# Performance work log

Measured on AMD Instinct MI355X. Metric: run time of the kernel, lower is better.

Reference implementation:

```python
import jax, jax.numpy as jnp
import numpy as np

EMBED_DIM = 1024
NUM_HEADS = 16
HEAD_DIM = EMBED_DIM // NUM_HEADS


def setup_inputs() -> dict:
    key = jax.random.key(0)
    ks = jax.random.split(key, 12)
    B, S, D = 4, 2048, EMBED_DIM
    scale = 1.0 / np.sqrt(D)
    inp = {
        "query": jax.random.normal(ks[0], (B, S, D), jnp.float32),
        "key": jax.random.normal(ks[1], (B, S, D), jnp.float32),
        "value": jax.random.normal(ks[2], (B, S, D), jnp.float32),
        # nn.Linear weights: [out_features, in_features], y = x @ W.T + b
        "Wq": jax.random.normal(ks[3], (D, D), jnp.float32) * scale,
        "bq": jnp.zeros((D,), jnp.float32),
        "Wk": jax.random.normal(ks[4], (D, D), jnp.float32) * scale,
        "bk": jnp.zeros((D,), jnp.float32),
        "Wv": jax.random.normal(ks[5], (D, D), jnp.float32) * scale,
        "bv": jnp.zeros((D,), jnp.float32),
        "Wo": jax.random.normal(ks[6], (D, D), jnp.float32) * scale,
        "bo": jnp.zeros((D,), jnp.float32),
    }
    return inp


def reference(query, key, value, Wq, bq, Wk, bk, Wv, bv, Wo, bo):
    B, Sq, D = query.shape
    Sk = key.shape[1]
    H, Dh = NUM_HEADS, HEAD_DIM

    def proj(x, W, b):
        # [B,S,D] -> [B,H,S,Dh]
        y = jnp.einsum('bsd,ed->bse', x, W) + b
        return y.reshape(x.shape[0], x.shape[1], H, Dh).transpose(0, 2, 1, 3)

    q = proj(query, Wq, bq)
    k = proj(key, Wk, bk)
    v = proj(value, Wv, bv)

    # sigmoid attention (no softmax); dropout is identity in eval mode
    scores = jnp.einsum('bhqd,bhkd->bhqk', q, k) / jnp.sqrt(jnp.float32(Dh)).astype(q.dtype)
    attn = jax.nn.sigmoid(scores)
    out = jnp.einsum('bhqk,bhkd->bhqd', attn, v)

    out = out.transpose(0, 2, 1, 3).reshape(B, Sq, D)
    return jnp.einsum('bsd,ed->bse', out, Wo) + bo
```

## Files before the change

### kernel.cpp

```cpp
#include <hip/hip_runtime.h>


typedef _Float16 f16x2 __attribute__((ext_vector_type(2)));
typedef _Float16 f16x4 __attribute__((ext_vector_type(4)));
typedef _Float16 f16x8 __attribute__((ext_vector_type(8)));
typedef __fp16   h16x2 __attribute__((ext_vector_type(2)));
typedef float    f32x4 __attribute__((ext_vector_type(4)));
typedef float    f32x16 __attribute__((ext_vector_type(16)));

typedef __attribute__((address_space(3))) void* lds_vp;
typedef const __attribute__((address_space(1))) void* gbl_vp;

__device__ __forceinline__ void gld_lds16(const void* g, void* l) {
  __builtin_amdgcn_global_load_lds((gbl_vp)g, (lds_vp)l, 16, 0, 0);
}

__device__ __forceinline__ f16x8 cvt8(float4 a, float4 b) {
  return (f16x8){(_Float16)a.x, (_Float16)a.y, (_Float16)a.z, (_Float16)a.w,
                 (_Float16)b.x, (_Float16)b.y, (_Float16)b.z, (_Float16)b.w};
}

__device__ __forceinline__ f16x2 pk2(float a, float b) {
  h16x2 r = __builtin_amdgcn_cvt_pkrtz(a, b);
  return __builtin_bit_cast(f16x2, r);
}

#define BM 128
#define BN 128
#define BK 32

template <bool AF16, bool BF16, bool TRANSV, bool OUTF32>
__global__ __launch_bounds__(256) void gemm_bt(const void* __restrict__ Av,
                                               const void* __restrict__ Bv,
                                               const float* __restrict__ bias,
                                               void* __restrict__ Yv,
                                               int M, int N, int K) {
  __shared__ __align__(16) _Float16 sA[BM * BK];
  __shared__ __align__(16) _Float16 sB[BN * BK];

  const int t = threadIdx.x, lane = t & 63, wid = t >> 6;
  const int m0 = blockIdx.x * BM, n0 = blockIdx.y * BN;
  const int wm = (wid >> 1) * 64, wn = (wid & 1) * 64;
  const int lrow = lane & 15, g = lane >> 4;

  f32x4 acc[4][4] = {};

  const int arow = 16 * wid + (lane >> 2);
  const int gq = (lane & 3) ^ ((lane >> 3) & 3);
  _Float16* lA1 = sA + wid * 512;
  _Float16* lA2 = sA + 2048 + wid * 512;
  _Float16* lB1 = sB + wid * 512;
  _Float16* lB2 = sB + 2048 + wid * 512;

  const int mrow = t >> 1, mhalf = t & 1;
  const int mm = (mrow >> 1) & 3;
  const int ch_lo = mrow * 4 + ((2 * mhalf) ^ mm);
  const int ch_hi = ch_lo ^ 1;

  const _Float16* pA16a = nullptr; const _Float16* pA16b = nullptr;
  const float* pA32 = nullptr;
  if constexpr (AF16) {
    const _Float16* A = (const _Float16*)Av;
    pA16a = A + (size_t)(m0 + arow) * K + gq * 8;
    pA16b = A + (size_t)(m0 + 64 + arow) * K + gq * 8;
  } else {
    pA32 = (const float*)Av + (size_t)(m0 + mrow) * K + mhalf * 16;
  }
  const _Float16* pB16a = nullptr; const _Float16* pB16b = nullptr;
  const float* pB32 = nullptr;
  if constexpr (BF16) {
    const _Float16* B = (const _Float16*)Bv;
    pB16a = B + (size_t)(n0 + arow) * K + gq * 8;
    pB16b = B + (size_t)(n0 + 64 + arow) * K + gq * 8;
  } else {
    pB32 = (const float*)Bv + (size_t)(n0 + mrow) * K + mhalf * 16;
  }

  const int xr = g ^ ((lrow >> 1) & 3);

  for (int k0 = 0; k0 < K; k0 += BK) {
    float4 av[4], bv4[4];
    if constexpr (!AF16) {
      const float4* p = (const float4*)(pA32 + k0);
      av[0] = p[0]; av[1] = p[1]; av[2] = p[2]; av[3] = p[3];
    }
    if constexpr (!BF16) {
      const float4* p = (const float4*)(pB32 + k0);
      bv4[0] = p[0]; bv4[1] = p[1]; bv4[2] = p[2]; bv4[3] = p[3];
    }
    __syncthreads();
    if constexpr (AF16) {
      gld_lds16(pA16a + k0, lA1);
      gld_lds16(pA16b + k0, lA2);
    } else {
      *(f16x8*)(sA + ch_lo * 8) = cvt8(av[0], av[1]);
      *(f16x8*)(sA + ch_hi * 8) = cvt8(av[2], av[3]);
    }
    if constexpr (BF16) {
      gld_lds16(pB16a + k0, lB1);
      gld_lds16(pB16b + k0, lB2);
    } else {
      *(f16x8*)(sB + ch_lo * 8) = cvt8(bv4[0], bv4[1]);
      *(f16x8*)(sB + ch_hi * 8) = cvt8(bv4[2], bv4[3]);
    }
    __syncthreads();

    f16x8 af[4], bf[4];
#pragma unroll
    for (int i = 0; i < 4; i++)
      af[i] = *(const f16x8*)(sA + (wm + i * 16 + lrow) * 32 + xr * 8);
#pragma unroll
    for (int j = 0; j < 4; j++)
      bf[j] = *(const f16x8*)(sB + (wn + j * 16 + lrow) * 32 + xr * 8);
#pragma unroll
    for (int i = 0; i < 4; i++)
#pragma unroll
      for (int j = 0; j < 4; j++)
        acc[i][j] = __builtin_amdgcn_mfma_f32_16x16x32_f16(af[i], bf[j], acc[i][j], 0, 0, 0);
  }

  const int orow = g * 4, ocol = lrow;
#pragma unroll
  for (int j = 0; j < 4; j++) {
    const int col = n0 + wn + j * 16 + ocol;
    const float bv = bias[col];
#pragma unroll
    for (int i = 0; i < 4; i++) {
      const int row = m0 + wm + i * 16 + orow;
      if constexpr (TRANSV) {
        _Float16* VT = (_Float16*)Yv;
        int s = row & 2047;
        int sp = (s & ~12) | ((s & 4) << 1) | ((s & 8) >> 1);
        _Float16* dst = VT + (((size_t)(row >> 11) * 16 + (col >> 6)) * 64 + (col & 63)) * 2048 + sp;
        f16x4 v = {(_Float16)(acc[i][j][0] + bv), (_Float16)(acc[i][j][1] + bv),
                   (_Float16)(acc[i][j][2] + bv), (_Float16)(acc[i][j][3] + bv)};
        *(f16x4*)dst = v;
      } else if constexpr (OUTF32) {
        float* Y = (float*)Yv;
#pragma unroll
        for (int r = 0; r < 4; r++) Y[(size_t)(row + r) * N + col] = acc[i][j][r] + bv;
      } else {
        _Float16* Y = (_Float16*)Yv;
#pragma unroll
        for (int r = 0; r < 4; r++) Y[(size_t)(row + r) * N + col] = (_Float16)(acc[i][j][r] + bv);
      }
    }
  }
}

__global__ __launch_bounds__(256) void qkv_gemm(const _Float16* __restrict__ Xq,
                                                const _Float16* __restrict__ Xk,
                                                const _Float16* __restrict__ Xv,
                                                const _Float16* __restrict__ W,
                                                const float* __restrict__ bq,
                                                const float* __restrict__ bk,
                                                const float* __restrict__ bv,
                                                _Float16* __restrict__ Qo,
                                                _Float16* __restrict__ Ko,
                                                _Float16* __restrict__ VT) {
  __shared__ __align__(16) _Float16 sA[BM * BK];
  __shared__ __align__(16) _Float16 sB[BN * BK];

  const int t = threadIdx.x, lane = t & 63, wid = t >> 6;
  const int n0g = blockIdx.x * BN, m0 = blockIdx.y * BM;
  const int seg = blockIdx.x >> 3, n0 = n0g & 1023;
  const _Float16* A = (seg == 0) ? Xq : (seg == 1) ? Xk : Xv;
  const float* bias = (seg == 0) ? bq : (seg == 1) ? bk : bv;
  const int K = 1024;

  const int wm = (wid >> 1) * 64, wn = (wid & 1) * 64;
  const int lrow = lane & 15, g = lane >> 4;

  f32x4 acc[4][4] = {};

  const int arow = 16 * wid + (lane >> 2);
  const int gq = (lane & 3) ^ ((lane >> 3) & 3);
  _Float16* lA1 = sA + wid * 512;
  _Float16* lA2 = sA + 2048 + wid * 512;
  _Float16* lB1 = sB + wid * 512;
  _Float16* lB2 = sB + 2048 + wid * 512;

  const _Float16* pA16a = A + (size_t)(m0 + arow) * K + gq * 8;
  const _Float16* pA16b = A + (size_t)(m0 + 64 + arow) * K + gq * 8;
  const _Float16* pB16a = W + (size_t)(n0g + arow) * K + gq * 8;
  const _Float16* pB16b = W + (size_t)(n0g + 64 + arow) * K + gq * 8;

  const int xr = g ^ ((lrow >> 1) & 3);

  for (int k0 = 0; k0 < K; k0 += BK) {
    __syncthreads();
    gld_lds16(pA16a + k0, lA1);
    gld_lds16(pA16b + k0, lA2);
    gld_lds16(pB16a + k0, lB1);
    gld_lds16(pB16b + k0, lB2);
    __syncthreads();

    f16x8 af[4], bf[4];
#pragma unroll
    for (int i = 0; i < 4; i++)
      af[i] = *(const f16x8*)(sA + (wm + i * 16 + lrow) * 32 + xr * 8);
#pragma unroll
    for (int j = 0; j < 4; j++)
      bf[j] = *(const f16x8*)(sB + (wn + j * 16 + lrow) * 32 + xr * 8);
#pragma unroll
    for (int i = 0; i < 4; i++)
#pragma unroll
      for (int j = 0; j < 4; j++)
        acc[i][j] = __builtin_amdgcn_mfma_f32_16x16x32_f16(af[i], bf[j], acc[i][j], 0, 0, 0);
  }

  const int orow = g * 4, ocol = lrow;
#pragma unroll
  for (int j = 0; j < 4; j++) {
    const int col = n0 + wn + j * 16 + ocol;
    const float bvv = bias[col];
#pragma unroll
    for (int i = 0; i < 4; i++) {
      const int row = m0 + wm + i * 16 + orow;
      if (seg == 2) {
        int s = row & 2047;
        int sp = (s & ~12) | ((s & 4) << 1) | ((s & 8) >> 1);
        _Float16* dst = VT + (((size_t)(row >> 11) * 16 + (col >> 6)) * 64 + (col & 63)) * 2048 + sp;
        f16x4 v = {(_Float16)(acc[i][j][0] + bvv), (_Float16)(acc[i][j][1] + bvv),
                   (_Float16)(acc[i][j][2] + bvv), (_Float16)(acc[i][j][3] + bvv)};
        *(f16x4*)dst = v;
      } else {
        _Float16* Y = (seg == 0) ? Qo : Ko;
#pragma unroll
        for (int r = 0; r < 4; r++) Y[(size_t)(row + r) * 1024 + col] = (_Float16)(acc[i][j][r] + bvv);
      }
    }
  }
}

#define LDS_ROW 72

__global__ __launch_bounds__(256, 4) void attn_sig(const _Float16* __restrict__ Q,
                                                   const _Float16* __restrict__ K,
                                                   const _Float16* __restrict__ VT,
                                                   _Float16* __restrict__ O) {
  __shared__ __align__(16) _Float16 smem[128 * LDS_ROW];
  _Float16* sK = smem;
  _Float16* sVT = smem + 64 * LDS_ROW;

  const int t = threadIdx.x, lane = t & 63, wid = t >> 6;
  const int l31 = lane & 31, g5 = lane >> 5;
  const int b = blockIdx.z, h = blockIdx.y, q0 = blockIdx.x * 128;
  const int qw = q0 + wid * 32;

  f16x8 qf[4];
  {
    const _Float16* qp = Q + (size_t)(b * 2048 + qw + l31) * 1024 + h * 64;
#pragma unroll
    for (int dhc = 0; dhc < 4; dhc++)
      qf[dhc] = *(const f16x8*)(qp + dhc * 16 + g5 * 8) * (_Float16)-0.125f;
  }

  f32x16 oacc[2] = {};

  const int srow = t >> 2, scol = (t & 3) * 16;
  const _Float16* kbase = K + ((size_t)(b * 2048) + srow) * 1024 + h * 64 + scol;
  const _Float16* vbase = VT + ((size_t)((b * 16 + h) * 64 + srow)) * 2048 + scol;

  uint4 ka = *(const uint4*)kbase;
  uint4 kb = *(const uint4*)(kbase + 8);
  uint4 va = *(const uint4*)vbase;
  uint4 vb = *(const uint4*)(vbase + 8);

  for (int kt = 0; kt < 2048; kt += 64) {
    __syncthreads();
    *(uint4*)&sK[srow * LDS_ROW + scol] = ka;
    *(uint4*)&sK[srow * LDS_ROW + scol + 8] = kb;
    *(uint4*)&sVT[srow * LDS_ROW + scol] = va;
    *(uint4*)&sVT[srow * LDS_ROW + scol + 8] = vb;
    __syncthreads();

    const int kt2 = kt + 64;
    if (kt2 < 2048) {
      ka = *(const uint4*)(kbase + (size_t)kt2 * 1024);
      kb = *(const uint4*)(kbase + (size_t)kt2 * 1024 + 8);
      va = *(const uint4*)(vbase + kt2);
      vb = *(const uint4*)(vbase + kt2 + 8);
    }

#pragma unroll
    for (int kt32 = 0; kt32 < 2; kt32++) {
      f16x8 kf[4];
#pragma unroll
      for (int dhc = 0; dhc < 4; dhc++)
        kf[dhc] = *(const f16x8*)&sK[(kt32 * 32 + l31) * LDS_ROW + dhc * 16 + g5 * 8];

      f32x16 sacc = {};
#pragma unroll
      for (int dhc = 0; dhc < 4; dhc++)
        sacc = __builtin_amdgcn_mfma_f32_32x32x16_f16(kf[dhc], qf[dhc], sacc, 0, 0, 0);

      f16x8 pf[2];
#pragma unroll
      for (int G = 0; G < 2; G++) {
        union { f16x8 v; f16x2 h[4]; } u;
#pragma unroll
        for (int pr = 0; pr < 4; pr++) {
          float e0 = __expf(sacc[G * 8 + pr * 2 + 0]);
          float e1 = __expf(sacc[G * 8 + pr * 2 + 1]);
          u.h[pr] = pk2(__builtin_amdgcn_rcpf(1.0f + e0),
                        __builtin_amdgcn_rcpf(1.0f + e1));
        }
        pf[G] = u.v;
      }

#pragma unroll
      for (int dht = 0; dht < 2; dht++)
#pragma unroll
        for (int G = 0; G < 2; G++) {
          f16x8 vf = *(const f16x8*)&sVT[(dht * 32 + l31) * LDS_ROW + kt32 * 32 + G * 16 + g5 * 8];
          oacc[dht] = __builtin_amdgcn_mfma_f32_32x32x16_f16(vf, pf[G], oacc[dht], 0, 0, 0);
        }
    }
  }

  __syncthreads();
  _Float16* ep = smem;
#pragma unroll
  for (int dht = 0; dht < 2; dht++)
#pragma unroll
    for (int c = 0; c < 4; c++) {
      f16x4 o4 = {(_Float16)oacc[dht][4 * c + 0], (_Float16)oacc[dht][4 * c + 1],
                  (_Float16)oacc[dht][4 * c + 2], (_Float16)oacc[dht][4 * c + 3]};
      *(f16x4*)&ep[(wid * 32 + l31) * LDS_ROW + dht * 32 + c * 8 + g5 * 4] = o4;
    }
  __syncthreads();
#pragma unroll
  for (int i = 0; i < 4; i++) {
    const int q = i * 32 + (t >> 3), dhc = t & 7;
    f16x8 row = *(const f16x8*)&ep[q * LDS_ROW + dhc * 8];
    *(f16x8*)(O + (size_t)(b * 2048 + q0 + q) * 1024 + h * 64 + dhc * 8) = row;
  }
}

struct CvtArgs {
  const float* src[7];
  _Float16* dst[7];
  int n[7];
  int cnt;
};

__global__ __launch_bounds__(256) void cvt_f32_f16(CvtArgs a) {
  const int ti = blockIdx.y;
  if (ti >= a.cnt) return;
  const int i = (blockIdx.x * 256 + threadIdx.x) * 8;
  if (i >= a.n[ti]) return;
  const float4* s = (const float4*)(a.src[ti] + i);
  float4 x = s[0], y = s[1];
  *(f16x8*)(a.dst[ti] + i) = cvt8(x, y);
}

extern "C" void kernel_launch(void* const* d_in, const int* in_sizes, int n_in,
                              void* d_out, int out_size, void* d_ws, size_t ws_size,
                              hipStream_t stream) {
  const float* query = (const float*)d_in[0];
  const float* key   = (const float*)d_in[1];
  const float* value = (const float*)d_in[2];
  const float* Wq = (const float*)d_in[3];
  const float* bq = (const float*)d_in[4];
  const float* Wk = (const float*)d_in[5];
  const float* bk = (const float*)d_in[6];
  const float* Wv = (const float*)d_in[7];
  const float* bv = (const float*)d_in[8];
  const float* Wo = (const float*)d_in[9];
  const float* bo = (const float*)d_in[10];
  float* out = (float*)d_out;

  const int D = 1024, M = 8192;
  const size_t MB = 1024 * 1024;
  char* ws = (char*)d_ws;
  dim3 bb(256), ga(16, 16, 4);

  if (ws_size >= 104 * MB) {
    _Float16* Xq = (_Float16*)(ws + 0 * MB);
    _Float16* Xk = (_Float16*)(ws + 16 * MB);
    _Float16* Xv = (_Float16*)(ws + 32 * MB);
    _Float16* Qp = (_Float16*)(ws + 48 * MB);
    _Float16* Kp = (_Float16*)(ws + 64 * MB);
    _Float16* VT = (_Float16*)(ws + 80 * MB);
    _Float16* Wf = (_Float16*)(ws + 96 * MB);
    _Float16* AO = Xq;
    CvtArgs ca{};
    ca.src[0] = query; ca.dst[0] = Xq; ca.n[0] = M * D;
    ca.src[1] = key;   ca.dst[1] = Xk; ca.n[1] = M * D;
    ca.src[2] = value; ca.dst[2] = Xv; ca.n[2] = M * D;
    ca.src[3] = Wq; ca.dst[3] = Wf + 0 * 1048576; ca.n[3] = D * D;
    ca.src[4] = Wk; ca.dst[4] = Wf + 1 * 1048576; ca.n[4] = D * D;
    ca.src[5] = Wv; ca.dst[5] = Wf + 2 * 1048576; ca.n[5] = D * D;
    ca.src[6] = Wo; ca.dst[6] = Wf + 3 * 1048576; ca.n[6] = D * D;
    ca.cnt = 7;
    cvt_f32_f16<<<dim3(4096, 7), bb, 0, stream>>>(ca);
    qkv_gemm<<<dim3(24, 64), bb, 0, stream>>>(Xq, Xk, Xv, Wf, bq, bk, bv, Qp, Kp, VT);
    attn_sig<<<ga, bb, 0, stream>>>(Qp, Kp, VT, AO);
    gemm_bt<true, true, false, true><<<dim3(64, 8), bb, 0, stream>>>(AO, Wf + 3 * 1048576, bo, out, M, D, D);
  } else {
    _Float16* Qp = (_Float16*)(ws + 0 * MB);
    _Float16* Kp = (_Float16*)(ws + 16 * MB);
    _Float16* VT = (_Float16*)(ws + 32 * MB);
    _Float16* AO = (_Float16*)(ws + 48 * MB);
    gemm_bt<false, false, false, false><<<dim3(64, 8), bb, 0, stream>>>(query, Wq, bq, Qp, M, D, D);
    gemm_bt<false, false, false, false><<<dim3(64, 8), bb, 0, stream>>>(key,   Wk, bk, Kp, M, D, D);
    gemm_bt<false, false, true,  false><<<dim3(64, 8), bb, 0, stream>>>(value, Wv, bv, VT, M, D, D);
    attn_sig<<<ga, bb, 0, stream>>>(Qp, Kp, VT, AO);
    gemm_bt<true, false, false, true><<<dim3(64, 8), bb, 0, stream>>>(AO, Wo, bo, out, M, D, D);
  }
}
```

Measured before the change: 374.3 us.

## Split attention over key halves, use exp2 with prescaled Q, add MFMA priority

Splits the key dimension of the sigmoid attention into two halves, each block writing a partial output that a new add kernel sums before the output projection. Folds log2(e) into the Q scale so the sigmoid uses a raw exp2 instruction, and raises wave priority around MFMA sections. This aims to improve occupancy and balance, and trims per-element exp work. The cost is extra partial-output traffic and an additional kernel launch.

```diff
diff --git a/kernel.cpp b/kernel.cpp
--- a/kernel.cpp
+++ b/kernel.cpp
@@ -23,6 +23,16 @@
 __device__ __forceinline__ f16x2 pk2(float a, float b) {
   h16x2 r = __builtin_amdgcn_cvt_pkrtz(a, b);
   return __builtin_bit_cast(f16x2, r);
+}
+
+__device__ __forceinline__ float exp2_fast(float x) {
+#if __has_builtin(__builtin_amdgcn_exp2f)
+  return __builtin_amdgcn_exp2f(x);
+#else
+  float r;
+  asm("v_exp_f32 %0, %1" : "=v"(r) : "v"(x));
+  return r;
+#endif
 }
 
 #define BM 128
@@ -235,6 +245,7 @@
 
 #define LDS_ROW 72
 
+template <int KSPL>
 __global__ __launch_bounds__(256, 4) void attn_sig(const _Float16* __restrict__ Q,
                                                    const _Float16* __restrict__ K,
                                                    const _Float16* __restrict__ VT,
@@ -243,9 +254,14 @@
   _Float16* sK = smem;
   _Float16* sVT = smem + 64 * LDS_ROW;
 
+  constexpr int SKEY = 2048 / KSPL;
+
   const int t = threadIdx.x, lane = t & 63, wid = t >> 6;
   const int l31 = lane & 31, g5 = lane >> 5;
-  const int b = blockIdx.z, h = blockIdx.y, q0 = blockIdx.x * 128;
+  const int b = blockIdx.z, h = blockIdx.y;
+  const int qb = (KSPL == 2) ? (int)(blockIdx.x >> 1) : (int)blockIdx.x;
+  const int kh = (KSPL == 2) ? (int)(blockIdx.x & 1) : 0;
+  const int q0 = qb * 128;
   const int qw = q0 + wid * 32;
 
   f16x8 qf[4];
@@ -253,21 +269,21 @@
     const _Float16* qp = Q + (size_t)(b * 2048 + qw + l31) * 1024 + h * 64;
 #pragma unroll
     for (int dhc = 0; dhc < 4; dhc++)
-      qf[dhc] = *(const f16x8*)(qp + dhc * 16 + g5 * 8) * (_Float16)-0.125f;
+      qf[dhc] = *(const f16x8*)(qp + dhc * 16 + g5 * 8) * (_Float16)-0.18033688f;
   }
 
   f32x16 oacc[2] = {};
 
   const int srow = t >> 2, scol = (t & 3) * 16;
-  const _Float16* kbase = K + ((size_t)(b * 2048) + srow) * 1024 + h * 64 + scol;
-  const _Float16* vbase = VT + ((size_t)((b * 16 + h) * 64 + srow)) * 2048 + scol;
+  const _Float16* kbase = K + ((size_t)(b * 2048) + kh * SKEY + srow) * 1024 + h * 64 + scol;
+  const _Float16* vbase = VT + ((size_t)((b * 16 + h) * 64 + srow)) * 2048 + kh * SKEY + scol;
 
   uint4 ka = *(const uint4*)kbase;
   uint4 kb = *(const uint4*)(kbase + 8);
   uint4 va = *(const uint4*)vbase;
   uint4 vb = *(const uint4*)(vbase + 8);
 
-  for (int kt = 0; kt < 2048; kt += 64) {
+  for (int kt = 0; kt < SKEY; kt += 64) {
     __syncthreads();
     *(uint4*)&sK[srow * LDS_ROW + scol] = ka;
     *(uint4*)&sK[srow * LDS_ROW + scol + 8] = kb;
@@ -276,7 +292,7 @@
     __syncthreads();
 
     const int kt2 = kt + 64;
-    if (kt2 < 2048) {
+    if (kt2 < SKEY) {
       ka = *(const uint4*)(kbase + (size_t)kt2 * 1024);
       kb = *(const uint4*)(kbase + (size_t)kt2 * 1024 + 8);
       va = *(const uint4*)(vbase + kt2);
@@ -291,9 +307,11 @@
         kf[dhc] = *(const f16x8*)&sK[(kt32 * 32 + l31) * LDS_ROW + dhc * 16 + g5 * 8];
 
       f32x16 sacc = {};
+      __builtin_amdgcn_s_setprio(1);
 #pragma unroll
       for (int dhc = 0; dhc < 4; dhc++)
         sacc = __builtin_amdgcn_mfma_f32_32x32x16_f16(kf[dhc], qf[dhc], sacc, 0, 0, 0);
+      __builtin_amdgcn_s_setprio(0);
 
       f16x8 pf[2];
 #pragma unroll
@@ -301,14 +319,15 @@
         union { f16x8 v; f16x2 h[4]; } u;
 #pragma unroll
         for (int pr = 0; pr < 4; pr++) {
-          float e0 = __expf(sacc[G * 8 + pr * 2 + 0]);
-          float e1 = __expf(sacc[G * 8 + pr * 2 + 1]);
+          float e0 = exp2_fast(sacc[G * 8 + pr * 2 + 0]);
+          float e1 = exp2_fast(sacc[G * 8 + pr * 2 + 1]);
           u.h[pr] = pk2(__builtin_amdgcn_rcpf(1.0f + e0),
                         __builtin_amdgcn_rcpf(1.0f + e1));
         }
         pf[G] = u.v;
       }
 
+      __builtin_amdgcn_s_setprio(1);
 #pragma unroll
       for (int dht = 0; dht < 2; dht++)
 #pragma unroll
@@ -316,9 +335,11 @@
           f16x8 vf = *(const f16x8*)&sVT[(dht * 32 + l31) * LDS_ROW + kt32 * 32 + G * 16 + g5 * 8];
           oacc[dht] = __builtin_amdgcn_mfma_f32_32x32x16_f16(vf, pf[G], oacc[dht], 0, 0, 0);
         }
-    }
-  }
-
+      __builtin_amdgcn_s_setprio(0);
+    }
+  }
+
+  _Float16* Ob = O + (size_t)kh * (8192 * 1024);
   __syncthreads();
   _Float16* ep = smem;
 #pragma unroll
@@ -334,8 +355,18 @@
   for (int i = 0; i < 4; i++) {
     const int q = i * 32 + (t >> 3), dhc = t & 7;
     f16x8 row = *(const f16x8*)&ep[q * LDS_ROW + dhc * 8];
-    *(f16x8*)(O + (size_t)(b * 2048 + q0 + q) * 1024 + h * 64 + dhc * 8) = row;
-  }
+    *(f16x8*)(Ob + (size_t)(b * 2048 + q0 + q) * 1024 + h * 64 + dhc * 8) = row;
+  }
+}
+
+__global__ __launch_bounds__(256) void add_halves(const _Float16* __restrict__ a,
+                                                  const _Float16* __restrict__ b,
+                                                  _Float16* __restrict__ o, int n) {
+  const int i = (blockIdx.x * 256 + threadIdx.x) * 8;
+  if (i >= n) return;
+  f16x8 x = *(const f16x8*)(a + i);
+  f16x8 y = *(const f16x8*)(b + i);
+  *(f16x8*)(o + i) = x + y;
 }
 
 struct CvtArgs {
@@ -374,7 +405,7 @@
   const int D = 1024, M = 8192;
   const size_t MB = 1024 * 1024;
   char* ws = (char*)d_ws;
-  dim3 bb(256), ga(16, 16, 4);
+  dim3 bb(256);
 
   if (ws_size >= 104 * MB) {
     _Float16* Xq = (_Float16*)(ws + 0 * MB);
@@ -384,7 +415,9 @@
     _Float16* Kp = (_Float16*)(ws + 64 * MB);
     _Float16* VT = (_Float16*)(ws + 80 * MB);
     _Float16* Wf = (_Float16*)(ws + 96 * MB);
-    _Float16* AO = Xq;
+    _Float16* AO0 = Xq;
+    _Float16* AO1 = Xk;
+    _Float16* AO  = Xv;
     CvtArgs ca{};
     ca.src[0] = query; ca.dst[0] = Xq; ca.n[0] = M * D;
     ca.src[1] = key;   ca.dst[1] = Xk; ca.n[1] = M * D;
@@ -396,7 +429,8 @@
     ca.cnt = 7;
     cvt_f32_f16<<<dim3(4096, 7), bb, 0, stream>>>(ca);
     qkv_gemm<<<dim3(24, 64), bb, 0, stream>>>(Xq, Xk, Xv, Wf, bq, bk, bv, Qp, Kp, VT);
-    attn_sig<<<ga, bb, 0, stream>>>(Qp, Kp, VT, AO);
+    attn_sig<2><<<dim3(32, 16, 4), bb, 0, stream>>>(Qp, Kp, VT, AO0);
+    add_halves<<<dim3(4096), bb, 0, stream>>>(AO0, AO1, AO, M * D);
     gemm_bt<true, true, false, true><<<dim3(64, 8), bb, 0, stream>>>(AO, Wf + 3 * 1048576, bo, out, M, D, D);
   } else {
     _Float16* Qp = (_Float16*)(ws + 0 * MB);
@@ -406,7 +440,7 @@
     gemm_bt<false, false, false, false><<<dim3(64, 8), bb, 0, stream>>>(query, Wq, bq, Qp, M, D, D);
     gemm_bt<false, false, false, false><<<dim3(64, 8), bb, 0, stream>>>(key,   Wk, bk, Kp, M, D, D);
     gemm_bt<false, false, true,  false><<<dim3(64, 8), bb, 0, stream>>>(value, Wv, bv, VT, M, D, D);
-    attn_sig<<<ga, bb, 0, stream>>>(Qp, Kp, VT, AO);
+    attn_sig<1><<<dim3(16, 16, 4), bb, 0, stream>>>(Qp, Kp, VT, AO);
     gemm_bt<true, false, false, true><<<dim3(64, 8), bb, 0, stream>>>(AO, Wo, bo, out, M, D, D);
   }
 }
```

New measurement: 369.2 us. About the same (-1.4%).

## Double-buffer attention K/V tiles and software-pipeline PV MFMAs with exp2 sigmoid

Applied to the files above, without the earlier changes.

The sigmoid attention kernel now keeps two LDS buffers for K/VT tiles, so each tile iteration needs one barrier instead of two. The second chunk's PV MFMA is deferred into the next iteration so it can overlap the barrier and the following QK work. The exp is replaced by a raw exp2 with the log2(e) factor folded into the Q scale. This costs double the LDS and more registers, and occupancy is lowered to 3 blocks per CU.

```diff
diff --git a/kernel.cpp b/kernel.cpp
--- a/kernel.cpp
+++ b/kernel.cpp
@@ -23,6 +23,16 @@
 __device__ __forceinline__ f16x2 pk2(float a, float b) {
   h16x2 r = __builtin_amdgcn_cvt_pkrtz(a, b);
   return __builtin_bit_cast(f16x2, r);
+}
+
+__device__ __forceinline__ float exp2_fast(float x) {
+#if __has_builtin(__builtin_amdgcn_exp2f)
+  return __builtin_amdgcn_exp2f(x);
+#else
+  float r;
+  asm("v_exp_f32 %0, %1" : "=v"(r) : "v"(x));
+  return r;
+#endif
 }
 
 #define BM 128
@@ -234,26 +244,26 @@
 }
 
 #define LDS_ROW 72
-
-__global__ __launch_bounds__(256, 4) void attn_sig(const _Float16* __restrict__ Q,
+#define TILE_E (64 * LDS_ROW)
+
+__global__ __launch_bounds__(256, 3) void attn_sig(const _Float16* __restrict__ Q,
                                                    const _Float16* __restrict__ K,
                                                    const _Float16* __restrict__ VT,
                                                    _Float16* __restrict__ O) {
-  __shared__ __align__(16) _Float16 smem[128 * LDS_ROW];
-  _Float16* sK = smem;
-  _Float16* sVT = smem + 64 * LDS_ROW;
+  __shared__ __align__(16) _Float16 smem[4 * TILE_E];
 
   const int t = threadIdx.x, lane = t & 63, wid = t >> 6;
   const int l31 = lane & 31, g5 = lane >> 5;
   const int b = blockIdx.z, h = blockIdx.y, q0 = blockIdx.x * 128;
   const int qw = q0 + wid * 32;
+  const int NT = 32;
 
   f16x8 qf[4];
   {
     const _Float16* qp = Q + (size_t)(b * 2048 + qw + l31) * 1024 + h * 64;
 #pragma unroll
     for (int dhc = 0; dhc < 4; dhc++)
-      qf[dhc] = *(const f16x8*)(qp + dhc * 16 + g5 * 8) * (_Float16)-0.125f;
+      qf[dhc] = *(const f16x8*)(qp + dhc * 16 + g5 * 8) * (_Float16)-0.18033688f;
   }
 
   f32x16 oacc[2] = {};
@@ -262,62 +272,110 @@
   const _Float16* kbase = K + ((size_t)(b * 2048) + srow) * 1024 + h * 64 + scol;
   const _Float16* vbase = VT + ((size_t)((b * 16 + h) * 64 + srow)) * 2048 + scol;
 
-  uint4 ka = *(const uint4*)kbase;
-  uint4 kb = *(const uint4*)(kbase + 8);
-  uint4 va = *(const uint4*)vbase;
-  uint4 vb = *(const uint4*)(vbase + 8);
-
-  for (int kt = 0; kt < 2048; kt += 64) {
-    __syncthreads();
-    *(uint4*)&sK[srow * LDS_ROW + scol] = ka;
-    *(uint4*)&sK[srow * LDS_ROW + scol + 8] = kb;
-    *(uint4*)&sVT[srow * LDS_ROW + scol] = va;
-    *(uint4*)&sVT[srow * LDS_ROW + scol + 8] = vb;
-    __syncthreads();
-
-    const int kt2 = kt + 64;
-    if (kt2 < 2048) {
-      ka = *(const uint4*)(kbase + (size_t)kt2 * 1024);
-      kb = *(const uint4*)(kbase + (size_t)kt2 * 1024 + 8);
-      va = *(const uint4*)(vbase + kt2);
-      vb = *(const uint4*)(vbase + kt2 + 8);
-    }
-
-#pragma unroll
-    for (int kt32 = 0; kt32 < 2; kt32++) {
-      f16x8 kf[4];
-#pragma unroll
-      for (int dhc = 0; dhc < 4; dhc++)
-        kf[dhc] = *(const f16x8*)&sK[(kt32 * 32 + l31) * LDS_ROW + dhc * 16 + g5 * 8];
-
-      f32x16 sacc = {};
-#pragma unroll
-      for (int dhc = 0; dhc < 4; dhc++)
-        sacc = __builtin_amdgcn_mfma_f32_32x32x16_f16(kf[dhc], qf[dhc], sacc, 0, 0, 0);
-
-      f16x8 pf[2];
-#pragma unroll
-      for (int G = 0; G < 2; G++) {
-        union { f16x8 v; f16x2 h[4]; } u;
-#pragma unroll
-        for (int pr = 0; pr < 4; pr++) {
-          float e0 = __expf(sacc[G * 8 + pr * 2 + 0]);
-          float e1 = __expf(sacc[G * 8 + pr * 2 + 1]);
-          u.h[pr] = pk2(__builtin_amdgcn_rcpf(1.0f + e0),
-                        __builtin_amdgcn_rcpf(1.0f + e1));
-        }
-        pf[G] = u.v;
-      }
-
-#pragma unroll
-      for (int dht = 0; dht < 2; dht++)
-#pragma unroll
-        for (int G = 0; G < 2; G++) {
-          f16x8 vf = *(const f16x8*)&sVT[(dht * 32 + l31) * LDS_ROW + kt32 * 32 + G * 16 + g5 * 8];
-          oacc[dht] = __builtin_amdgcn_mfma_f32_32x32x16_f16(vf, pf[G], oacc[dht], 0, 0, 0);
-        }
-    }
-  }
+#define LOAD_TILE(tile)                                                  \
+  ka = *(const uint4*)(kbase + (size_t)(tile) * 64 * 1024);              \
+  kb = *(const uint4*)(kbase + (size_t)(tile) * 64 * 1024 + 8);          \
+  va = *(const uint4*)(vbase + (tile) * 64);                             \
+  vb = *(const uint4*)(vbase + (tile) * 64 + 8);
+
+#define WRITE_TILE(p)                                                    \
+  {                                                                      \
+    _Float16* dK = smem + (p) * 2 * TILE_E;                              \
+    _Float16* dV = dK + TILE_E;                                          \
+    *(uint4*)&dK[srow * LDS_ROW + scol] = ka;                            \
+    *(uint4*)&dK[srow * LDS_ROW + scol + 8] = kb;                        \
+    *(uint4*)&dV[srow * LDS_ROW + scol] = va;                            \
+    *(uint4*)&dV[srow * LDS_ROW + scol + 8] = vb;                        \
+  }
+
+#define QK_CHUNK(sacc, sKp, c)                                           \
+  {                                                                      \
+    _Float16* sk_ = (sKp);                                               \
+    f16x8 kf0 = *(const f16x8*)&sk_[((c) * 32 + l31) * LDS_ROW + 0 * 16 + g5 * 8];  \
+    f16x8 kf1 = *(const f16x8*)&sk_[((c) * 32 + l31) * LDS_ROW + 1 * 16 + g5 * 8];  \
+    f16x8 kf2 = *(const f16x8*)&sk_[((c) * 32 + l31) * LDS_ROW + 2 * 16 + g5 * 8];  \
+    f16x8 kf3 = *(const f16x8*)&sk_[((c) * 32 + l31) * LDS_ROW + 3 * 16 + g5 * 8];  \
+    sacc = __builtin_amdgcn_mfma_f32_32x32x16_f16(kf0, qf[0], sacc, 0, 0, 0);       \
+    sacc = __builtin_amdgcn_mfma_f32_32x32x16_f16(kf1, qf[1], sacc, 0, 0, 0);       \
+    sacc = __builtin_amdgcn_mfma_f32_32x32x16_f16(kf2, qf[2], sacc, 0, 0, 0);       \
+    sacc = __builtin_amdgcn_mfma_f32_32x32x16_f16(kf3, qf[3], sacc, 0, 0, 0);       \
+  }
+
+#define PACK_PF(pf, sacc)                                                \
+  {                                                                      \
+    _Pragma("unroll")                                                    \
+    for (int G = 0; G < 2; G++) {                                        \
+      union { f16x8 v; f16x2 hh[4]; } u;                                 \
+      _Pragma("unroll")                                                  \
+      for (int pr = 0; pr < 4; pr++) {                                   \
+        float e0 = exp2_fast(sacc[G * 8 + pr * 2 + 0]);                  \
+        float e1 = exp2_fast(sacc[G * 8 + pr * 2 + 1]);                  \
+        u.hh[pr] = pk2(__builtin_amdgcn_rcpf(1.0f + e0),                 \
+                       __builtin_amdgcn_rcpf(1.0f + e1));                \
+      }                                                                  \
+      pf[G] = u.v;                                                       \
+    }                                                                    \
+  }
+
+#define VF_READ(vf, sVp, c)                                              \
+  {                                                                      \
+    _Float16* sv_ = (sVp);                                               \
+    vf[0][0] = *(const f16x8*)&sv_[(0 * 32 + l31) * LDS_ROW + (c) * 32 + 0 * 16 + g5 * 8]; \
+    vf[0][1] = *(const f16x8*)&sv_[(0 * 32 + l31) * LDS_ROW + (c) * 32 + 1 * 16 + g5 * 8]; \
+    vf[1][0] = *(const f16x8*)&sv_[(1 * 32 + l31) * LDS_ROW + (c) * 32 + 0 * 16 + g5 * 8]; \
+    vf[1][1] = *(const f16x8*)&sv_[(1 * 32 + l31) * LDS_ROW + (c) * 32 + 1 * 16 + g5 * 8]; \
+  }
+
+#define PV_ACC(vf, pf)                                                   \
+  oacc[0] = __builtin_amdgcn_mfma_f32_32x32x16_f16(vf[0][0], pf[0], oacc[0], 0, 0, 0); \
+  oacc[0] = __builtin_amdgcn_mfma_f32_32x32x16_f16(vf[0][1], pf[1], oacc[0], 0, 0, 0); \
+  oacc[1] = __builtin_amdgcn_mfma_f32_32x32x16_f16(vf[1][0], pf[0], oacc[1], 0, 0, 0); \
+  oacc[1] = __builtin_amdgcn_mfma_f32_32x32x16_f16(vf[1][1], pf[1], oacc[1], 0, 0, 0);
+
+  uint4 ka, kb, va, vb;
+  f16x8 pfA[2], pfP[2];
+  f16x8 vfA[2][2], vfP[2][2];
+  f32x16 saccA, saccB;
+
+  LOAD_TILE(0);
+  WRITE_TILE(0);
+
+  {
+    _Float16* sKp = smem;
+    _Float16* sVp = smem + TILE_E;
+    __syncthreads();
+    LOAD_TILE(1);
+    saccA = (f32x16){};
+    QK_CHUNK(saccA, sKp, 0);
+    saccB = (f32x16){};
+    QK_CHUNK(saccB, sKp, 1);
+    PACK_PF(pfA, saccA);
+    VF_READ(vfA, sVp, 0);
+    PV_ACC(vfA, pfA);
+    PACK_PF(pfP, saccB);
+    VF_READ(vfP, sVp, 1);
+    WRITE_TILE(1);
+  }
+
+  for (int tt = 1; tt < NT; ++tt) {
+    const int p = tt & 1;
+    _Float16* sKp = smem + p * 2 * TILE_E;
+    _Float16* sVp = sKp + TILE_E;
+    __syncthreads();
+    PV_ACC(vfP, pfP);
+    if (tt + 1 < NT) { LOAD_TILE(tt + 1); }
+    saccA = (f32x16){};
+    QK_CHUNK(saccA, sKp, 0);
+    saccB = (f32x16){};
+    QK_CHUNK(saccB, sKp, 1);
+    PACK_PF(pfA, saccA);
+    VF_READ(vfA, sVp, 0);
+    PV_ACC(vfA, pfA);
+    PACK_PF(pfP, saccB);
+    VF_READ(vfP, sVp, 1);
+    if (tt + 1 < NT) { WRITE_TILE(p ^ 1); }
+  }
+  PV_ACC(vfP, pfP);
 
   __syncthreads();
   _Float16* ep = smem;
@@ -374,7 +432,7 @@
   const int D = 1024, M = 8192;
   const size_t MB = 1024 * 1024;
   char* ws = (char*)d_ws;
-  dim3 bb(256), ga(16, 16, 4);
+  dim3 bb(256);
 
   if (ws_size >= 104 * MB) {
     _Float16* Xq = (_Float16*)(ws + 0 * MB);
@@ -396,7 +454,7 @@
     ca.cnt = 7;
     cvt_f32_f16<<<dim3(4096, 7), bb, 0, stream>>>(ca);
     qkv_gemm<<<dim3(24, 64), bb, 0, stream>>>(Xq, Xk, Xv, Wf, bq, bk, bv, Qp, Kp, VT);
-    attn_sig<<<ga, bb, 0, stream>>>(Qp, Kp, VT, AO);
+    attn_sig<<<dim3(16, 16, 4), bb, 0, stream>>>(Qp, Kp, VT, AO);
     gemm_bt<true, true, false, true><<<dim3(64, 8), bb, 0, stream>>>(AO, Wf + 3 * 1048576, bo, out, M, D, D);
   } else {
     _Float16* Qp = (_Float16*)(ws + 0 * MB);
@@ -406,7 +464,7 @@
     gemm_bt<false, false, false, false><<<dim3(64, 8), bb, 0, stream>>>(query, Wq, bq, Qp, M, D, D);
     gemm_bt<false, false, false, false><<<dim3(64, 8), bb, 0, stream>>>(key,   Wk, bk, Kp, M, D, D);
     gemm_bt<false, false, true,  false><<<dim3(64, 8), bb, 0, stream>>>(value, Wv, bv, VT, M, D, D);
-    attn_sig<<<ga, bb, 0, stream>>>(Qp, Kp, VT, AO);
+    attn_sig<<<dim3(16, 16, 4), bb, 0, stream>>>(Qp, Kp, VT, AO);
     gemm_bt<true, false, false, true><<<dim3(64, 8), bb, 0, stream>>>(AO, Wo, bo, out, M, D, D);
   }
 }
```

Result: no change. 370.8 us (-0.9%).
